# Kernel tuning notes

Hardware: AMD Instinct MI355X
Metric: run time of the kernel (lower is better)

The kernel has to match this reference:

```python
import jax, jax.numpy as jnp
import numpy as np

N = 50000
E = 800000
IN_CH = 128
HID = 64
OUT_CH = 1
HEADS = 2


def setup_inputs() -> dict:
    key = jax.random.key(0)
    k1, k2, k3, k4, k5, k6, k7 = jax.random.split(key, 7)
    x = jax.random.normal(k1, (N, IN_CH), dtype=jnp.float32)
    row = jax.random.randint(k2, (E,), 0, N)
    col = jax.random.randint(k3, (E,), 0, N)
    edge_index = jnp.stack([row, col], axis=0).astype(jnp.int64)
    # Xavier-uniform-ish init scales
    def xavier(k, shape):
        fan_in, fan_out = shape[0], shape[1]
        lim = float(np.sqrt(6.0 / (fan_in + fan_out)))
        return jax.random.uniform(k, shape, jnp.float32, -lim, lim)
    W0 = xavier(k4, (IN_CH, HEADS * HID))          # layer 0 lin weight (transposed torch layout)
    attn0 = xavier(k5, (HEADS, 2 * HID))
    W1 = xavier(k6, (HID, HEADS * OUT_CH))         # layer 1 lin weight
    attn1 = xavier(k7, (HEADS, 2 * OUT_CH))
    return {"x": x, "edge_index": edge_index, "W0": W0, "attn0": attn0, "W1": W1, "attn1": attn1}


def _segment_softmax(alpha, row, num_nodes):
    # alpha: [E, H]; per-target-node (row) softmax across incoming edges.
    m = jax.ops.segment_max(alpha, row, num_segments=num_nodes)   # [N, H]
    ex = jnp.exp(alpha - m[row])
    s = jax.ops.segment_sum(ex, row, num_segments=num_nodes)      # [N, H]
    return ex / s[row]


def _gat_layer(x, edge_index, W, attn, heads, out_ch):
    n = x.shape[0]
    h = (x @ W).reshape(n, heads, out_ch)                         # [N, H, C]
    row, col = edge_index[0], edge_index[1]
    h_row = h[row]                                                # [E, H, C]
    h_col = h[col]                                                # [E, H, C]
    # (cat([h_row,h_col]) * attn).sum(-1) split into two contractions
    alpha = (jnp.einsum('ehc,hc->eh', h_row, attn[:, :out_ch])
             + jnp.einsum('ehc,hc->eh', h_col, attn[:, out_ch:]))
    alpha = jax.nn.leaky_relu(alpha, negative_slope=0.2)
    alpha = _segment_softmax(alpha, row, n)                        # [E, H]
    out = jax.ops.segment_sum(alpha[..., None] * h_col, row, num_segments=n)  # [N, H, C]
    return out.mean(axis=1), alpha


def reference(x, edge_index, W0, attn0, W1, attn1):
    h, _ = _gat_layer(x, edge_index, W0, attn0, HEADS, HID)
    h = jax.nn.relu(h)
    out, attn = _gat_layer(h, edge_index, W1, attn1, HEADS, OUT_CH)
    return out  # [N, OUT_CH]
```

## Files before the change

kernel.cpp:

```cpp
#include <hip/hip_runtime.h>
#include <math.h>

#define NNODES 50000
#define NEDGES 800000
#define NBKT 196
#define BKT_CAP 5120
#define EPB 2048
#define NBA ((NEDGES + EPB - 1) / EPB)
#define NBN ((NNODES + 63) / 64)

typedef __attribute__((ext_vector_type(8))) short short8;
typedef __attribute__((ext_vector_type(4))) float f32x4;

__device__ inline float bsum64(float v) {
    #pragma unroll
    for (int off = 1; off < 64; off <<= 1) v += __shfl_xor(v, off, 64);
    return v;
}

__device__ inline unsigned packbf2(float a, float b) {
    unsigned ua = __float_as_uint(a);
    unsigned ub = __float_as_uint(b);
    ua = (ua + 0x7fffu + ((ua >> 16) & 1u)) >> 16;
    ub = (ub + 0x7fffu + ((ub >> 16) & 1u)) >> 16;
    return ua | (ub << 16);
}
__device__ inline float bflo(unsigned u) { return __uint_as_float(u << 16); }
__device__ inline float bfhi(unsigned u) { return __uint_as_float(u & 0xffff0000u); }

__global__ __launch_bounds__(256) void k_prep(const float* __restrict__ W,
                                              unsigned short* __restrict__ Whi,
                                              unsigned short* __restrict__ Wlo,
                                              int* __restrict__ gcur) {
    if (blockIdx.x == 64) {
        int i = threadIdx.x;
        if (i < NBKT) gcur[i] = 0;
        return;
    }
    int tid = blockIdx.x * 256 + threadIdx.x;
    int i = tid & 7, lane = (tid >> 3) & 63, ct = (tid >> 9) & 7, kc = tid >> 12;
    int k = kc * 32 + (lane >> 4) * 8 + i;
    int col = ct * 16 + (lane & 15);
    float v = W[k * 128 + col];
    unsigned hb = packbf2(v, 0.f) & 0xffffu;
    float hv = __uint_as_float(hb << 16);
    unsigned lb = packbf2(v - hv, 0.f) & 0xffffu;
    Whi[tid] = (unsigned short)hb;
    Wlo[tid] = (unsigned short)lb;
}

__global__ __launch_bounds__(256) void k_nodeA(const int* __restrict__ ei,
                                               int* __restrict__ gcur,
                                               unsigned* __restrict__ stag,
                                               const float* __restrict__ x,
                                               const unsigned short* __restrict__ Whi,
                                               const unsigned short* __restrict__ Wlo,
                                               const float* __restrict__ attn0,
                                               float* __restrict__ ar,
                                               float* __restrict__ ac,
                                               unsigned* __restrict__ h0b) {
    __shared__ int lh[NBKT];
    __shared__ int lbase[NBKT];
    int t = threadIdx.x;

    if (blockIdx.x < NBA) {
        for (int i = t; i < NBKT; i += 256) lh[i] = 0;
        __syncthreads();
        int e0 = blockIdx.x * EPB;
        int rows[8], cols[8];
        #pragma unroll
        for (int i = 0; i < 8; i++) {
            int e = e0 + i * 256 + t;
            if (e < NEDGES) {
                rows[i] = ei[e];
                cols[i] = ei[NEDGES + e];
                atomicAdd(&lh[rows[i] >> 8], 1);
            }
        }
        __syncthreads();
        for (int i = t; i < NBKT; i += 256) {
            lbase[i] = atomicAdd(&gcur[i], lh[i]);
            lh[i] = 0;
        }
        __syncthreads();
        #pragma unroll
        for (int i = 0; i < 8; i++) {
            int e = e0 + i * 256 + t;
            if (e < NEDGES) {
                int b = rows[i] >> 8;
                int rank = atomicAdd(&lh[b], 1);
                stag[b * BKT_CAP + lbase[b] + rank] =
                    ((unsigned)(rows[i] & 255) << 16) | (unsigned)cols[i];
            }
        }
        return;
    }

    int bid = blockIdx.x - NBA;
    int w = t >> 6, lane = t & 63;
    int n0 = bid * 64 + w * 16;
    int c16 = lane & 15, grp = lane >> 4;
    int arow = n0 + c16;
    bool rowok = arow < NNODES;

    f32x4 acc[8];
    #pragma unroll
    for (int ct = 0; ct < 8; ct++) acc[ct] = (f32x4){0.f, 0.f, 0.f, 0.f};

    const uint4* WH = (const uint4*)Whi;
    const uint4* WL = (const uint4*)Wlo;

    for (int kc = 0; kc < 4; kc++) {
        float xv[8];
        if (rowok) {
            *(float4*)&xv[0] = *(const float4*)&x[arow * 128 + kc * 32 + grp * 8];
            *(float4*)&xv[4] = *(const float4*)&x[arow * 128 + kc * 32 + grp * 8 + 4];
        } else {
            #pragma unroll
            for (int i = 0; i < 8; i++) xv[i] = 0.f;
        }
        unsigned ah[4], al[4];
        #pragma unroll
        for (int i = 0; i < 4; i++) ah[i] = packbf2(xv[2 * i], xv[2 * i + 1]);
        #pragma unroll
        for (int i = 0; i < 4; i++) {
            float l0 = xv[2 * i] - bflo(ah[i]);
            float l1 = xv[2 * i + 1] - bfhi(ah[i]);
            al[i] = packbf2(l0, l1);
        }
        short8 a_h = *(short8*)ah;
        short8 a_l = *(short8*)al;

        #pragma unroll
        for (int ct = 0; ct < 8; ct++) {
            uint4 whv = WH[(kc * 8 + ct) * 64 + lane];
            uint4 wlv = WL[(kc * 8 + ct) * 64 + lane];
            short8 b_h = *(short8*)&whv;
            short8 b_l = *(short8*)&wlv;
            acc[ct] = __builtin_amdgcn_mfma_f32_16x16x32_bf16(a_h, b_h, acc[ct], 0, 0, 0);
            acc[ct] = __builtin_amdgcn_mfma_f32_16x16x32_bf16(a_h, b_l, acc[ct], 0, 0, 0);
            acc[ct] = __builtin_amdgcn_mfma_f32_16x16x32_bf16(a_l, b_h, acc[ct], 0, 0, 0);
        }
    }

    #pragma unroll
    for (int reg = 0; reg < 4; reg++) {
        float pr0 = 0.f, pc0 = 0.f, pr1 = 0.f, pc1 = 0.f;
        #pragma unroll
        for (int ct = 0; ct < 4; ct++) {
            float v = acc[ct][reg];
            int ch = ct * 16 + c16;
            pr0 += v * attn0[ch];
            pc0 += v * attn0[64 + ch];
        }
        #pragma unroll
        for (int ct = 4; ct < 8; ct++) {
            float v = acc[ct][reg];
            int ch = (ct - 4) * 16 + c16;
            pr1 += v * attn0[128 + ch];
            pc1 += v * attn0[192 + ch];
        }
        #pragma unroll
        for (int off = 1; off < 16; off <<= 1) {
            pr0 += __shfl_xor(pr0, off, 64);
            pc0 += __shfl_xor(pc0, off, 64);
            pr1 += __shfl_xor(pr1, off, 64);
            pc1 += __shfl_xor(pc1, off, 64);
        }
        int n = n0 + grp * 4 + reg;
        if (c16 == 0 && n < NNODES) {
            ar[n * 2] = pr0;     ac[n * 2] = pc0;
            ar[n * 2 + 1] = pr1; ac[n * 2 + 1] = pc1;
        }
    }

    #pragma unroll
    for (int reg = 0; reg < 4; reg++) {
        int n = n0 + grp * 4 + reg;
        if (n < NNODES) {
            #pragma unroll
            for (int ct = 0; ct < 4; ct++)
                h0b[n * 64 + ct * 16 + c16] = packbf2(acc[ct][reg], acc[ct + 4][reg]);
        }
    }
}

__global__ __launch_bounds__(256) void k_binC(const int* __restrict__ gcur,
                                              const unsigned* __restrict__ stag,
                                              int* __restrict__ rowptr,
                                              int* __restrict__ ecol) {
    __shared__ int sh[256];
    __shared__ int dg[256];
    __shared__ int sc[256];
    __shared__ int cur[256];
    __shared__ int lout[BKT_CAP];
    int b = blockIdx.x, t = threadIdx.x;
    int gv = (t < NBKT) ? gcur[t] : 0;
    sh[t] = gv;
    __syncthreads();
    #pragma unroll
    for (int off = 1; off < 256; off <<= 1) {
        int u = (t >= off) ? sh[t - off] : 0;
        __syncthreads();
        sh[t] += u;
        __syncthreads();
    }
    int cnt = gcur[b];
    int base = sh[b] - cnt;
    dg[t] = 0;
    __syncthreads();
    for (int i = t; i < cnt; i += 256)
        atomicAdd(&dg[stag[b * BKT_CAP + i] >> 16], 1);
    __syncthreads();
    int v = dg[t];
    sc[t] = v;
    __syncthreads();
    #pragma unroll
    for (int off = 1; off < 256; off <<= 1) {
        int u = (t >= off) ? sc[t - off] : 0;
        __syncthreads();
        sc[t] += u;
        __syncthreads();
    }
    int excl = sc[t] - v;
    int gidx = b * 256 + t;
    if (gidx <= NNODES) rowptr[gidx] = base + excl;
    cur[t] = excl;
    __syncthreads();
    for (int i = t; i < cnt; i += 256) {
        unsigned p = stag[b * BKT_CAP + i];
        int pos = atomicAdd(&cur[p >> 16], 1);
        lout[pos] = (int)(p & 0xffffu);
    }
    __syncthreads();
    for (int i = t; i < cnt; i += 256) ecol[base + i] = lout[i];
}

__global__ __launch_bounds__(256) void k_l0edge(const int* __restrict__ rowptr,
                                                const int* __restrict__ ecol,
                                                const float* __restrict__ ar,
                                                const float* __restrict__ ac,
                                                const unsigned* __restrict__ h0b,
                                                const float* __restrict__ W1,
                                                float* __restrict__ h1) {
    int w = threadIdx.x >> 6, lane = threadIdx.x & 63;
    int n = blockIdx.x * 4 + w;
    if (n >= NNODES) return;
    int beg = rowptr[n];
    int deg = rowptr[n + 1] - beg;
    float arn0 = ar[n * 2], arn1 = ar[n * 2 + 1];
    int esub = lane >> 4;
    int c16 = lane & 15;
    float accA[4] = {0.f, 0.f, 0.f, 0.f};
    float accB[4] = {0.f, 0.f, 0.f, 0.f};
    float s0t = 0.f, s1t = 0.f;
    for (int wb = 0; wb < deg; wb += 64) {
        int cnt = deg - wb; if (cnt > 64) cnt = 64;
        float p0 = 0.f, p1 = 0.f; int colr = 0;
        if (lane < cnt) {
            colr = ecol[beg + wb + lane];
            float2 acv = ((const float2*)ac)[colr];
            float a0 = arn0 + acv.x, a1 = arn1 + acv.y;
            a0 = a0 > 0.f ? a0 : 0.2f * a0;
            a1 = a1 > 0.f ? a1 : 0.2f * a1;
            p0 = __expf(a0); p1 = __expf(a1);
            s0t += p0; s1t += p1;
        }
        int tmax = (cnt + 3) >> 2;
        for (int tt = 0; tt < tmax; tt++) {
            int i4 = tt * 4 + esub;
            int colx = __shfl(colr, i4, 64);
            float q0 = __shfl(p0, i4, 64);
            float q1 = __shfl(p1, i4, 64);
            if (i4 < cnt) {
                const uint4 u = *(const uint4*)(h0b + colx * 64 + c16 * 4);
                accA[0] += q0 * bflo(u.x); accB[0] += q1 * bfhi(u.x);
                accA[1] += q0 * bflo(u.y); accB[1] += q1 * bfhi(u.y);
                accA[2] += q0 * bflo(u.z); accB[2] += q1 * bfhi(u.z);
                accA[3] += q0 * bflo(u.w); accB[3] += q1 * bfhi(u.w);
            }
        }
    }
    float s0 = bsum64(s0t), s1 = bsum64(s1t);
    #pragma unroll
    for (int jj = 0; jj < 4; jj++) {
        accA[jj] += __shfl_xor(accA[jj], 16, 64);
        accA[jj] += __shfl_xor(accA[jj], 32, 64);
        accB[jj] += __shfl_xor(accB[jj], 16, 64);
        accB[jj] += __shfl_xor(accB[jj], 32, 64);
    }
    float si0 = deg ? 0.5f / s0 : 0.f;
    float si1 = deg ? 0.5f / s1 : 0.f;
    float pA = 0.f, pB = 0.f;
    #pragma unroll
    for (int jj = 0; jj < 4; jj++) {
        float o = si0 * accA[jj] + si1 * accB[jj];
        o = o > 0.f ? o : 0.f;
        float2 wv = ((const float2*)W1)[c16 * 4 + jj];
        pA += o * wv.x; pB += o * wv.y;
    }
    #pragma unroll
    for (int off = 1; off < 16; off <<= 1) {
        pA += __shfl_xor(pA, off, 64);
        pB += __shfl_xor(pB, off, 64);
    }
    if (lane == 0) { h1[n * 2] = pA; h1[n * 2 + 1] = pB; }
}

__global__ __launch_bounds__(256) void k_fused1(const int* __restrict__ rowptr,
                                                const int* __restrict__ ecol,
                                                const float* __restrict__ h1,
                                                const float* __restrict__ attn1,
                                                float* __restrict__ dout) {
    int w = threadIdx.x >> 6, lane = threadIdx.x & 63;
    int n = blockIdx.x * 4 + w;
    if (n >= NNODES) return;
    int beg = rowptr[n], end = rowptr[n + 1];
    if (beg == end) { if (lane == 0) dout[n] = 0.f; return; }
    float w01 = attn1[1], w11 = attn1[3];
    float base0 = attn1[0] * h1[n * 2];
    float base1 = attn1[2] * h1[n * 2 + 1];
    float s0 = 0.f, s1 = 0.f, acc0 = 0.f, acc1 = 0.f;
    for (int i = beg + lane; i < end; i += 64) {
        int col = ecol[i];
        float2 v = ((const float2*)h1)[col];
        float a0 = base0 + w01 * v.x;
        float a1 = base1 + w11 * v.y;
        a0 = a0 > 0.f ? a0 : 0.2f * a0;
        a1 = a1 > 0.f ? a1 : 0.2f * a1;
        float p0 = __expf(a0), p1 = __expf(a1);
        s0 += p0; acc0 += p0 * v.x;
        s1 += p1; acc1 += p1 * v.y;
    }
    s0 = bsum64(s0); s1 = bsum64(s1);
    acc0 = bsum64(acc0); acc1 = bsum64(acc1);
    if (lane == 0) dout[n] = 0.5f * (acc0 / s0 + acc1 / s1);
}

extern "C" void kernel_launch(void* const* d_in, const int* in_sizes, int n_in,
                              void* d_out, int out_size, void* d_ws, size_t ws_size,
                              hipStream_t stream) {
    const float* x     = (const float*)d_in[0];
    const int*   ei    = (const int*)d_in[1];
    const float* W0    = (const float*)d_in[2];
    const float* attn0 = (const float*)d_in[3];
    const float* W1    = (const float*)d_in[4];
    const float* attn1 = (const float*)d_in[5];
    float* dout = (float*)d_out;

    float* ws = (float*)d_ws;
    float*          ar     = ws;
    float*          ac     = ar + NNODES * 2;
    float*          h1     = ac + NNODES * 2;
    unsigned*       h0b    = (unsigned*)(h1 + NNODES * 2);
    unsigned short* Whi    = (unsigned short*)(h0b + NNODES * 64);
    unsigned short* Wlo    = Whi + 128 * 128;
    int*            gcur   = (int*)(Wlo + 128 * 128);
    int*            rowptr = gcur + NBKT;
    unsigned*       stag   = (unsigned*)(rowptr + NNODES + 1);
    int*            ecol   = (int*)(stag + NBKT * BKT_CAP);

    k_prep<<<65, 256, 0, stream>>>(W0, Whi, Wlo, gcur);
    k_nodeA<<<NBA + NBN, 256, 0, stream>>>(ei, gcur, stag, x, Whi, Wlo, attn0, ar, ac, h0b);
    k_binC<<<NBKT, 256, 0, stream>>>(gcur, stag, rowptr, ecol);
    k_l0edge<<<(NNODES + 3) / 4, 256, 0, stream>>>(rowptr, ecol, ar, ac, h0b, W1, h1);
    k_fused1<<<(NNODES + 3) / 4, 256, 0, stream>>>(rowptr, ecol, h1, attn1, dout);
}
```

Before: 98.25 us.

## Stage split-bf16 weights in LDS and give each wave two row tiles

In the node-GEMM blocks of k_nodeA, the hi and lo bf16 weight fragments (64 KB) are now copied cooperatively into a shared buffer once per block, and every wave reads its B operands from LDS instead of global memory. Each wave now handles 32 rows (two 16-row MFMA tiles) instead of 16, so each weight fragment is reused across two tiles, and the block count halves. The goal is less global and L2 weight traffic per node. In exchange, the 64 KB shared allocation applies to every block, including the edge-binning blocks, which limits occupancy, and the doubled accumulators raise register pressure.

```diff
diff --git a/kernel.cpp b/kernel.cpp
--- a/kernel.cpp
+++ b/kernel.cpp
@@ -7,7 +7,7 @@
 #define BKT_CAP 5120
 #define EPB 2048
 #define NBA ((NEDGES + EPB - 1) / EPB)
-#define NBN ((NNODES + 63) / 64)
+#define NBN ((NNODES + 127) / 128)
 
 typedef __attribute__((ext_vector_type(8))) short short8;
 typedef __attribute__((ext_vector_type(4))) float f32x4;
@@ -59,11 +59,12 @@
                                                float* __restrict__ ar,
                                                float* __restrict__ ac,
                                                unsigned* __restrict__ h0b) {
-    __shared__ int lh[NBKT];
-    __shared__ int lbase[NBKT];
+    __shared__ uint4 shbuf[4096];
     int t = threadIdx.x;
 
     if (blockIdx.x < NBA) {
+        int* lh = (int*)shbuf;
+        int* lbase = lh + NBKT;
         for (int i = t; i < NBKT; i += 256) lh[i] = 0;
         __syncthreads();
         int e0 = blockIdx.x * EPB;
@@ -97,90 +98,105 @@
     }
 
     int bid = blockIdx.x - NBA;
+    const uint4* WHg = (const uint4*)Whi;
+    const uint4* WLg = (const uint4*)Wlo;
+    #pragma unroll
+    for (int i = 0; i < 8; i++) shbuf[i * 256 + t] = WHg[i * 256 + t];
+    #pragma unroll
+    for (int i = 0; i < 8; i++) shbuf[2048 + i * 256 + t] = WLg[i * 256 + t];
+    __syncthreads();
+
     int w = t >> 6, lane = t & 63;
-    int n0 = bid * 64 + w * 16;
+    int n0 = bid * 128 + w * 32;
     int c16 = lane & 15, grp = lane >> 4;
-    int arow = n0 + c16;
-    bool rowok = arow < NNODES;
-
-    f32x4 acc[8];
-    #pragma unroll
-    for (int ct = 0; ct < 8; ct++) acc[ct] = (f32x4){0.f, 0.f, 0.f, 0.f};
-
-    const uint4* WH = (const uint4*)Whi;
-    const uint4* WL = (const uint4*)Wlo;
+
+    f32x4 acc[2][8];
+    #pragma unroll
+    for (int f = 0; f < 2; f++)
+        #pragma unroll
+        for (int ct = 0; ct < 8; ct++) acc[f][ct] = (f32x4){0.f, 0.f, 0.f, 0.f};
 
     for (int kc = 0; kc < 4; kc++) {
-        float xv[8];
-        if (rowok) {
-            *(float4*)&xv[0] = *(const float4*)&x[arow * 128 + kc * 32 + grp * 8];
-            *(float4*)&xv[4] = *(const float4*)&x[arow * 128 + kc * 32 + grp * 8 + 4];
-        } else {
-            #pragma unroll
-            for (int i = 0; i < 8; i++) xv[i] = 0.f;
-        }
-        unsigned ah[4], al[4];
-        #pragma unroll
-        for (int i = 0; i < 4; i++) ah[i] = packbf2(xv[2 * i], xv[2 * i + 1]);
-        #pragma unroll
-        for (int i = 0; i < 4; i++) {
-            float l0 = xv[2 * i] - bflo(ah[i]);
-            float l1 = xv[2 * i + 1] - bfhi(ah[i]);
-            al[i] = packbf2(l0, l1);
-        }
-        short8 a_h = *(short8*)ah;
-        short8 a_l = *(short8*)al;
+        short8 a_h[2], a_l[2];
+        #pragma unroll
+        for (int f = 0; f < 2; f++) {
+            int arow = n0 + f * 16 + c16;
+            float xv[8];
+            if (arow < NNODES) {
+                *(float4*)&xv[0] = *(const float4*)&x[arow * 128 + kc * 32 + grp * 8];
+                *(float4*)&xv[4] = *(const float4*)&x[arow * 128 + kc * 32 + grp * 8 + 4];
+            } else {
+                #pragma unroll
+                for (int i = 0; i < 8; i++) xv[i] = 0.f;
+            }
+            unsigned ah[4], al[4];
+            #pragma unroll
+            for (int i = 0; i < 4; i++) ah[i] = packbf2(xv[2 * i], xv[2 * i + 1]);
+            #pragma unroll
+            for (int i = 0; i < 4; i++) {
+                float l0 = xv[2 * i] - bflo(ah[i]);
+                float l1 = xv[2 * i + 1] - bfhi(ah[i]);
+                al[i] = packbf2(l0, l1);
+            }
+            a_h[f] = *(short8*)ah;
+            a_l[f] = *(short8*)al;
+        }
 
         #pragma unroll
         for (int ct = 0; ct < 8; ct++) {
-            uint4 whv = WH[(kc * 8 + ct) * 64 + lane];
-            uint4 wlv = WL[(kc * 8 + ct) * 64 + lane];
+            uint4 whv = shbuf[(kc * 8 + ct) * 64 + lane];
+            uint4 wlv = shbuf[2048 + (kc * 8 + ct) * 64 + lane];
             short8 b_h = *(short8*)&whv;
             short8 b_l = *(short8*)&wlv;
-            acc[ct] = __builtin_amdgcn_mfma_f32_16x16x32_bf16(a_h, b_h, acc[ct], 0, 0, 0);
-            acc[ct] = __builtin_amdgcn_mfma_f32_16x16x32_bf16(a_h, b_l, acc[ct], 0, 0, 0);
-            acc[ct] = __builtin_amdgcn_mfma_f32_16x16x32_bf16(a_l, b_h, acc[ct], 0, 0, 0);
-        }
-    }
-
-    #pragma unroll
-    for (int reg = 0; reg < 4; reg++) {
-        float pr0 = 0.f, pc0 = 0.f, pr1 = 0.f, pc1 = 0.f;
-        #pragma unroll
-        for (int ct = 0; ct < 4; ct++) {
-            float v = acc[ct][reg];
-            int ch = ct * 16 + c16;
-            pr0 += v * attn0[ch];
-            pc0 += v * attn0[64 + ch];
-        }
-        #pragma unroll
-        for (int ct = 4; ct < 8; ct++) {
-            float v = acc[ct][reg];
-            int ch = (ct - 4) * 16 + c16;
-            pr1 += v * attn0[128 + ch];
-            pc1 += v * attn0[192 + ch];
-        }
-        #pragma unroll
-        for (int off = 1; off < 16; off <<= 1) {
-            pr0 += __shfl_xor(pr0, off, 64);
-            pc0 += __shfl_xor(pc0, off, 64);
-            pr1 += __shfl_xor(pr1, off, 64);
-            pc1 += __shfl_xor(pc1, off, 64);
-        }
-        int n = n0 + grp * 4 + reg;
-        if (c16 == 0 && n < NNODES) {
-            ar[n * 2] = pr0;     ac[n * 2] = pc0;
-            ar[n * 2 + 1] = pr1; ac[n * 2 + 1] = pc1;
-        }
-    }
-
-    #pragma unroll
-    for (int reg = 0; reg < 4; reg++) {
-        int n = n0 + grp * 4 + reg;
-        if (n < NNODES) {
-            #pragma unroll
-            for (int ct = 0; ct < 4; ct++)
-                h0b[n * 64 + ct * 16 + c16] = packbf2(acc[ct][reg], acc[ct + 4][reg]);
+            #pragma unroll
+            for (int f = 0; f < 2; f++) {
+                acc[f][ct] = __builtin_amdgcn_mfma_f32_16x16x32_bf16(a_h[f], b_h, acc[f][ct], 0, 0, 0);
+                acc[f][ct] = __builtin_amdgcn_mfma_f32_16x16x32_bf16(a_h[f], b_l, acc[f][ct], 0, 0, 0);
+                acc[f][ct] = __builtin_amdgcn_mfma_f32_16x16x32_bf16(a_l[f], b_h, acc[f][ct], 0, 0, 0);
+            }
+        }
+    }
+
+    #pragma unroll
+    for (int f = 0; f < 2; f++) {
+        #pragma unroll
+        for (int reg = 0; reg < 4; reg++) {
+            float pr0 = 0.f, pc0 = 0.f, pr1 = 0.f, pc1 = 0.f;
+            #pragma unroll
+            for (int ct = 0; ct < 4; ct++) {
+                float v = acc[f][ct][reg];
+                int ch = ct * 16 + c16;
+                pr0 += v * attn0[ch];
+                pc0 += v * attn0[64 + ch];
+            }
+            #pragma unroll
+            for (int ct = 4; ct < 8; ct++) {
+                float v = acc[f][ct][reg];
+                int ch = (ct - 4) * 16 + c16;
+                pr1 += v * attn0[128 + ch];
+                pc1 += v * attn0[192 + ch];
+            }
+            #pragma unroll
+            for (int off = 1; off < 16; off <<= 1) {
+                pr0 += __shfl_xor(pr0, off, 64);
+                pc0 += __shfl_xor(pc0, off, 64);
+                pr1 += __shfl_xor(pr1, off, 64);
+                pc1 += __shfl_xor(pc1, off, 64);
+            }
+            int n = n0 + f * 16 + grp * 4 + reg;
+            if (c16 == 0 && n < NNODES) {
+                ar[n * 2] = pr0;     ac[n * 2] = pc0;
+                ar[n * 2 + 1] = pr1; ac[n * 2 + 1] = pc1;
+            }
+        }
+        #pragma unroll
+        for (int reg = 0; reg < 4; reg++) {
+            int n = n0 + f * 16 + grp * 4 + reg;
+            if (n < NNODES) {
+                #pragma unroll
+                for (int ct = 0; ct < 4; ct++)
+                    h0b[n * 64 + ct * 16 + c16] = packbf2(acc[f][ct][reg], acc[f][ct + 4][reg]);
+            }
         }
     }
 }
```

Measured after the change: 98.39 us. No clear change (+0.1%).

## Split layer-0 edge aggregation across two waves per node; drop low-order x MFMA

Applied to the files above, without the earlier changes.

The layer-0 gather kernel now gives each node two wavefronts. Each wave handles half of the 64 packed channels and eight edges per step, and the two partial projections are combined through shared memory behind a barrier. This is meant to raise parallelism and memory-level parallelism in the latency-bound gather, at the cost of redundant softmax-weight computation in both waves and a block-wide sync. Separately, the node GEMM drops the x-low-part bf16 correction MFMA. That cuts compute by a third but lowers the precision of h0 to roughly single bf16 for x.

```diff
diff --git a/kernel.cpp b/kernel.cpp
--- a/kernel.cpp
+++ b/kernel.cpp
@@ -119,17 +119,10 @@
             #pragma unroll
             for (int i = 0; i < 8; i++) xv[i] = 0.f;
         }
-        unsigned ah[4], al[4];
+        unsigned ah[4];
         #pragma unroll
         for (int i = 0; i < 4; i++) ah[i] = packbf2(xv[2 * i], xv[2 * i + 1]);
-        #pragma unroll
-        for (int i = 0; i < 4; i++) {
-            float l0 = xv[2 * i] - bflo(ah[i]);
-            float l1 = xv[2 * i + 1] - bfhi(ah[i]);
-            al[i] = packbf2(l0, l1);
-        }
         short8 a_h = *(short8*)ah;
-        short8 a_l = *(short8*)al;
 
         #pragma unroll
         for (int ct = 0; ct < 8; ct++) {
@@ -139,7 +132,6 @@
             short8 b_l = *(short8*)&wlv;
             acc[ct] = __builtin_amdgcn_mfma_f32_16x16x32_bf16(a_h, b_h, acc[ct], 0, 0, 0);
             acc[ct] = __builtin_amdgcn_mfma_f32_16x16x32_bf16(a_h, b_l, acc[ct], 0, 0, 0);
-            acc[ct] = __builtin_amdgcn_mfma_f32_16x16x32_bf16(a_l, b_h, acc[ct], 0, 0, 0);
         }
     }
 
@@ -243,14 +235,15 @@
                                                 const unsigned* __restrict__ h0b,
                                                 const float* __restrict__ W1,
                                                 float* __restrict__ h1) {
+    __shared__ float shp[4][2];
     int w = threadIdx.x >> 6, lane = threadIdx.x & 63;
-    int n = blockIdx.x * 4 + w;
-    if (n >= NNODES) return;
+    int n = blockIdx.x * 2 + (w >> 1);
+    int half = w & 1;
     int beg = rowptr[n];
     int deg = rowptr[n + 1] - beg;
     float arn0 = ar[n * 2], arn1 = ar[n * 2 + 1];
-    int esub = lane >> 4;
-    int c16 = lane & 15;
+    int esub = lane >> 3;
+    int cg = lane & 7;
     float accA[4] = {0.f, 0.f, 0.f, 0.f};
     float accB[4] = {0.f, 0.f, 0.f, 0.f};
     float s0t = 0.f, s1t = 0.f;
@@ -266,14 +259,14 @@
             p0 = __expf(a0); p1 = __expf(a1);
             s0t += p0; s1t += p1;
         }
-        int tmax = (cnt + 3) >> 2;
+        int tmax = (cnt + 7) >> 3;
         for (int tt = 0; tt < tmax; tt++) {
-            int i4 = tt * 4 + esub;
-            int colx = __shfl(colr, i4, 64);
-            float q0 = __shfl(p0, i4, 64);
-            float q1 = __shfl(p1, i4, 64);
-            if (i4 < cnt) {
-                const uint4 u = *(const uint4*)(h0b + colx * 64 + c16 * 4);
+            int i8 = tt * 8 + esub;
+            int colx = __shfl(colr, i8, 64);
+            float q0 = __shfl(p0, i8, 64);
+            float q1 = __shfl(p1, i8, 64);
+            if (i8 < cnt) {
+                const uint4 u = *(const uint4*)(h0b + colx * 64 + half * 32 + cg * 4);
                 accA[0] += q0 * bflo(u.x); accB[0] += q1 * bfhi(u.x);
                 accA[1] += q0 * bflo(u.y); accB[1] += q1 * bfhi(u.y);
                 accA[2] += q0 * bflo(u.z); accB[2] += q1 * bfhi(u.z);
@@ -284,8 +277,10 @@
     float s0 = bsum64(s0t), s1 = bsum64(s1t);
     #pragma unroll
     for (int jj = 0; jj < 4; jj++) {
+        accA[jj] += __shfl_xor(accA[jj], 8, 64);
         accA[jj] += __shfl_xor(accA[jj], 16, 64);
         accA[jj] += __shfl_xor(accA[jj], 32, 64);
+        accB[jj] += __shfl_xor(accB[jj], 8, 64);
         accB[jj] += __shfl_xor(accB[jj], 16, 64);
         accB[jj] += __shfl_xor(accB[jj], 32, 64);
     }
@@ -296,15 +291,20 @@
     for (int jj = 0; jj < 4; jj++) {
         float o = si0 * accA[jj] + si1 * accB[jj];
         o = o > 0.f ? o : 0.f;
-        float2 wv = ((const float2*)W1)[c16 * 4 + jj];
+        float2 wv = ((const float2*)W1)[half * 32 + cg * 4 + jj];
         pA += o * wv.x; pB += o * wv.y;
     }
     #pragma unroll
-    for (int off = 1; off < 16; off <<= 1) {
+    for (int off = 1; off < 8; off <<= 1) {
         pA += __shfl_xor(pA, off, 64);
         pB += __shfl_xor(pB, off, 64);
     }
-    if (lane == 0) { h1[n * 2] = pA; h1[n * 2 + 1] = pB; }
+    if (lane == 0) { shp[w][0] = pA; shp[w][1] = pB; }
+    __syncthreads();
+    if (half == 0 && lane == 0) {
+        h1[n * 2]     = shp[w][0] + shp[w + 1][0];
+        h1[n * 2 + 1] = shp[w][1] + shp[w + 1][1];
+    }
 }
 
 __global__ __launch_bounds__(256) void k_fused1(const int* __restrict__ rowptr,
@@ -363,6 +363,6 @@
     k_prep<<<65, 256, 0, stream>>>(W0, Whi, Wlo, gcur);
     k_nodeA<<<NBA + NBN, 256, 0, stream>>>(ei, gcur, stag, x, Whi, Wlo, attn0, ar, ac, h0b);
     k_binC<<<NBKT, 256, 0, stream>>>(gcur, stag, rowptr, ecol);
-    k_l0edge<<<(NNODES + 3) / 4, 256, 0, stream>>>(rowptr, ecol, ar, ac, h0b, W1, h1);
+    k_l0edge<<<NNODES / 2, 256, 0, stream>>>(rowptr, ecol, ar, ac, h0b, W1, h1);
     k_fused1<<<(NNODES + 3) / 4, 256, 0, stream>>>(rowptr, ecol, h1, attn1, dout);
 }
```

Result: slower. 119.8 us (+21.9%).
